# Kernel optimization log

Hardware: AMD Instinct MI355X
Metric: run time of the kernel (lower is better)

The kernel has to match this reference:

```python
import jax, jax.numpy as jnp
import numpy as np

EPS = 1e-3  # keras LayerNormalization default epsilon

def _ln(x, gamma, beta):
    m = jnp.mean(x, axis=-1, keepdims=True)
    v = jnp.var(x, axis=-1, keepdims=True)
    return gamma * (x - m) * jax.lax.rsqrt(v + EPS) + beta

def setup_inputs() -> dict:
    B, T, F, H = 256, 128, 4, 512  # T*F must equal H (skip-connection constraint in context GRN)
    D = T * F
    key = jax.random.key(0)
    ks = jax.random.split(key, 16)
    s = lambda fan: 1.0 / np.sqrt(fan)
    inp = {
        "inputs": jax.random.normal(ks[0], (B, T, F), jnp.float32),
        # context GRN (input dim D = T*F = H)
        "W1c": jax.random.normal(ks[1], (D, H), jnp.float32) * s(D),
        "b1c": jnp.zeros((H,), jnp.float32),
        "W2c": jax.random.normal(ks[2], (H, H), jnp.float32) * s(H),
        "b2c": jnp.zeros((H,), jnp.float32),
        "Wgc": jax.random.normal(ks[3], (H, H), jnp.float32) * s(H),
        "bgc": jnp.zeros((H,), jnp.float32),
        "gamma_c": jnp.ones((H,), jnp.float32),
        "beta_c": jnp.zeros((H,), jnp.float32),
        # softmax variable-selection head
        "Wsel": jax.random.normal(ks[4], (H, F), jnp.float32) * s(H),
        "bsel": jnp.zeros((F,), jnp.float32),
        # F per-variable GRNs, batched over leading F axis (input dim 1)
        "w1": jax.random.normal(ks[5], (F, H), jnp.float32),
        "b1": jnp.zeros((F, H), jnp.float32),
        "W2": jax.random.normal(ks[6], (F, H, H), jnp.float32) * s(H),
        "b2": jnp.zeros((F, H), jnp.float32),
        "Wg": jax.random.normal(ks[7], (F, H, H), jnp.float32) * s(H),
        "bg": jnp.zeros((F, H), jnp.float32),
        "gamma": jnp.ones((F, H), jnp.float32),
        "beta": jnp.zeros((F, H), jnp.float32),
    }
    return inp

def reference(inputs, W1c, b1c, W2c, b2c, Wgc, bgc, gamma_c, beta_c,
              Wsel, bsel, w1, b1, W2, b2, Wg, bg, gamma, beta):
    B, T, F = inputs.shape
    # ---- context GRN on flattened inputs (skip == flat since T*F == H) ----
    flat = inputs.reshape(B, T * F)
    x = jax.nn.elu(flat @ W1c + b1c)
    x = x @ W2c + b2c
    g = jax.nn.sigmoid(x @ Wgc + bgc)
    ctx = _ln(g * x + (1.0 - g) * flat, gamma_c, beta_c)
    # ---- softmax selection weights over variables ----
    sel = jax.nn.softmax(ctx @ Wsel + bsel)  # [B, F]
    # ---- per-variable GRNs, batched over F (input is scalar per variable) ----
    v = inputs[..., None]                              # [B,T,F,1] (skip path)
    x1 = jax.nn.elu(v * w1 + b1)                       # [B,T,F,H]
    x2 = jnp.einsum('btfh,fhk->btfk', x1, W2) + b2     # dense2
    gv = jax.nn.sigmoid(jnp.einsum('btfh,fhk->btfk', x2, Wg) + bg)
    gated = gv * x2 + (1.0 - gv) * v                   # skip broadcasts [B,T,F,1]
    tv = _ln(gated, gamma, beta)                       # [B,T,F,H]
    # ---- weighted sum over variables ----
    selected = jnp.einsum('btfh,bf->bth', tv, sel)     # [B,T,H]
    sel_weights = jnp.tile(sel[:, None, None, :], (1, T, 1, 1))  # [B,T,1,F]
    return selected, sel_weights
```

## Files before the change

kernel.cpp:

```cpp
#include <hip/hip_runtime.h>
#include <math.h>


#define H 512
#define NF 4
#define MTOT 32768

typedef unsigned short u16;
typedef unsigned int u32;
typedef __attribute__((ext_vector_type(8))) short short8;
typedef __attribute__((ext_vector_type(4))) float f32x4;
typedef __attribute__((ext_vector_type(4))) u32 u32x4;

__device__ __forceinline__ u16 f2bf(float x) {
  union { float f; u32 u; } v; v.f = x;
  return (u16)((v.u + 0x7fffu + ((v.u >> 16) & 1u)) >> 16);
}
__device__ __forceinline__ float bf2f(u32 h16) {
  union { u32 u; float f; } v; v.u = h16 << 16;
  return v.f;
}
__device__ __forceinline__ float elu_f(float x) {
  return x > 0.0f ? x : (__expf(x) - 1.0f);
}
__device__ __forceinline__ float sigmoid_f(float x) {
  return __builtin_amdgcn_rcpf(1.0f + __expf(-x));
}
__device__ __forceinline__ u32 cvtpk(float lo, float hi) {
  u32 r;
  asm("v_cvt_pk_bf16_f32 %0, %1, %2" : "=v"(r) : "v"(lo), "v"(hi));
  return r;
}
template <int CTRL>
__device__ __forceinline__ float dppadd(float v) {
  int t = __builtin_amdgcn_update_dpp(0, __float_as_int(v), CTRL, 0xF, 0xF, true);
  return v + __int_as_float(t);
}
__device__ __forceinline__ float red16(float v) {
  v = dppadd<0xB1>(v);
  v = dppadd<0x4E>(v);
  v = dppadd<0x141>(v);
  v = dppadd<0x140>(v);
  return v;
}

__device__ __forceinline__ void glld16(const void* g, void* l) {
  __builtin_amdgcn_global_load_lds(
      (const __attribute__((address_space(1))) u32*)(unsigned long long)(uintptr_t)g,
      (__attribute__((address_space(3))) u32*)(u32)(uintptr_t)l, 16, 0, 0);
}

#define MFMA16(a, b, c) __builtin_amdgcn_mfma_f32_16x16x32_bf16((a), (b), (c), 0, 0, 0)

__global__ __launch_bounds__(256)
void pack_weights(const float* __restrict__ W2, const float* __restrict__ Wg,
                  const float* __restrict__ W1c, const float* __restrict__ W2c,
                  const float* __restrict__ Wgc,
                  u16* __restrict__ W2p, u16* __restrict__ Wgp, u16* __restrict__ Cp) {
  int g = blockIdx.x * 256 + threadIdx.x;
  int r = g & 32767; int mat = g >> 15;
  if (mat >= 11) return;
  int lane = r & 63, nt = (r >> 6) & 31, kk = (r >> 11) & 15;
  const float* src; u16* dst;
  if (mat < 4)      { src = W2 + (size_t)mat * 262144;       dst = W2p + (size_t)mat * 262144; }
  else if (mat < 8) { src = Wg + (size_t)(mat - 4) * 262144; dst = Wgp + (size_t)(mat - 4) * 262144; }
  else              { src = (mat == 8 ? W1c : (mat == 9 ? W2c : Wgc));
                      dst = Cp + (size_t)(mat - 8) * 262144; }
  dst += (((size_t)kk * 32 + nt) * 64 + lane) * 8;
  int n  = nt * 16 + (lane & 15);
  int k0 = kk * 32 + (lane >> 4) * 8;
  short8 pk;
  #pragma unroll
  for (int j = 0; j < 8; ++j) pk[j] = (short)f2bf(src[(size_t)(k0 + j) * H + n]);
  *(short8*)dst = pk;
}

struct TileCtx {
  int tid, wid, lane, quad, col;
};


template <bool PREFETCH_TAIL>
__device__ __forceinline__ void gemm_kloop(const TileCtx& c, const u16* Wp,
                                           const u16* nextWp,
                                           u16* sA, u16* sB0, u16* sB1,
                                           f32x4 acc[4][2]) {
  #pragma unroll 1
  for (int kk = 0; kk < 16; ++kk) {
    if (kk < 15) {
      const u16* src = Wp + (kk + 1) * 16384 + c.tid * 8;
      u16* dst = (((kk + 1) & 1) ? sB1 : sB0) + c.tid * 8;
      glld16(src, dst);
      glld16(src + 8192, dst + 8192);
    } else if (PREFETCH_TAIL) {
      const u16* src = nextWp + c.tid * 8;
      glld16(src, sB0 + c.tid * 8);
      glld16(src + 8192, sB0 + c.tid * 8 + 8192);
    }
    const u16* bp = ((kk & 1) ? sB1 : sB0) + c.wid * 1024 + c.lane * 8;
    short8 bb0 = *(const short8*)(bp);
    short8 bb1 = *(const short8*)(bp + 512);
    const int kq = kk * 4 + c.quad;
    const int s0 = (kq ^ (c.col & 7)) * 8;
    short8 a0 = *(const short8*)&sA[(     c.col) * 512 + s0];
    short8 a1 = *(const short8*)&sA[(16 + c.col) * 512 + s0];
    short8 a2 = *(const short8*)&sA[(32 + c.col) * 512 + s0];
    short8 a3 = *(const short8*)&sA[(48 + c.col) * 512 + s0];
    acc[0][0] = MFMA16(a0, bb0, acc[0][0]); acc[0][1] = MFMA16(a0, bb1, acc[0][1]);
    acc[1][0] = MFMA16(a1, bb0, acc[1][0]); acc[1][1] = MFMA16(a1, bb1, acc[1][1]);
    acc[2][0] = MFMA16(a2, bb0, acc[2][0]); acc[2][1] = MFMA16(a2, bb1, acc[2][1]);
    acc[3][0] = MFMA16(a3, bb0, acc[3][0]); acc[3][1] = MFMA16(a3, bb1, acc[3][1]);
    __syncthreads();
  }
}

__device__ __forceinline__ void store_x2_pair(const TileCtx& c, u16* sA,
                                              int mt, int nt, u32 o01, u32 o23) {
  const bool even = (c.lane & 1) == 0;
  const u32 send = even ? o23 : o01;
  const u32 recv = (u32)__builtin_amdgcn_update_dpp(0, (int)send, 0xB1, 0xF, 0xF, true);
  const u32 hi = even ? recv : o23;
  const u32 lo = even ? o01 : recv;
  const u32 dlo = __builtin_amdgcn_perm(hi, lo, 0x05040100u);
  const u32 dhi = __builtin_amdgcn_perm(hi, lo, 0x07060302u);
  const int n  = c.wid * 32 + nt * 16 + c.col;
  const int np = n & ~1;
  const int mA = mt * 16 + c.quad * 4 + (even ? 0 : 2);
  const int iA = mA * 512 + ((((np >> 3) ^ (mA & 7)) << 3) + (np & 7));
  const int mB = mA + 1;
  const int iB = mB * 512 + ((((np >> 3) ^ (mB & 7)) << 3) + (np & 7));
  *(u32*)&sA[iA] = dlo;
  *(u32*)&sA[iB] = dhi;
}

__device__ __forceinline__ void ln_reduce(const TileCtx& c, float* sRedF,
                                          f32x4 acc[4][2]) {
  #pragma unroll
  for (int mt = 0; mt < 4; ++mt) {
    float rs[4], rq[4];
    #pragma unroll
    for (int reg = 0; reg < 4; ++reg) {
      rs[reg] = 0.f; rq[reg] = 0.f;
      #pragma unroll
      for (int nt = 0; nt < 2; ++nt) {
        const float gt = acc[mt][nt][reg];
        rs[reg] += gt; rq[reg] += gt * gt;
      }
      rs[reg] = red16(rs[reg]);
      rq[reg] = red16(rq[reg]);
    }
    if (c.col == 0) {
      #pragma unroll
      for (int reg = 0; reg < 4; ++reg) {
        const int m = mt * 16 + c.quad * 4 + reg;
        float2 sq; sq.x = rs[reg]; sq.y = rq[reg];
        *(float2*)&sRedF[m * 36 + c.wid * 2] = sq;
      }
    }
  }
  __syncthreads();
  if (c.tid < 64) {
    const int row = c.tid;
    float s = 0.f, q = 0.f;
    #pragma unroll
    for (int jj = 0; jj < 8; ++jj) {
      float4 v = *(float4*)&sRedF[row * 36 + jj * 4];
      s += v.x + v.z; q += v.y + v.w;
    }
    const float mu = s * (1.0f / H);
    const float rstd = rsqrtf(q * (1.0f / H) - mu * mu + 1e-3f);
    float2 mr; mr.x = mu; mr.y = rstd;
    *(float2*)&sRedF[2304 + row * 2] = mr;
  }
  __syncthreads();
}

__global__ __launch_bounds__(1024)
void ctx_mfma(const float* __restrict__ in,
              const u16* __restrict__ Cp,
              const float* __restrict__ b1c, const float* __restrict__ b2c,
              const float* __restrict__ bgc,
              const float* __restrict__ gamma_c, const float* __restrict__ beta_c,
              const float* __restrict__ Wsel, const float* __restrict__ bsel,
              float* __restrict__ sel_ws,
              float* __restrict__ selw_out)
{
  __shared__ __align__(16) u16 smem[65536];
  u16* const sA  = smem;
  u16* const sB0 = smem + 32768;
  u16* const sB1 = smem + 49152;
  float* const sRedF = (float*)smem;
  float* const sZ   = (float*)sB0;
  float* const sSel = (float*)sB0 + 1024;

  TileCtx c;
  c.tid = threadIdx.x; c.wid = c.tid >> 6; c.lane = c.tid & 63;
  c.quad = c.lane >> 4; c.col = c.lane & 15;
  const int b0 = blockIdx.x * 64;
  const u16* W1cp = Cp;
  const u16* W2cp = Cp + 262144;
  const u16* Wgcp = Cp + 524288;

  glld16(W1cp + c.tid * 8, sB0 + c.tid * 8);
  glld16(W1cp + c.tid * 8 + 8192, sB0 + c.tid * 8 + 8192);

  {
    const int m = c.tid >> 4;
    const int kb = (c.tid & 15) * 32;
    const float* rowp = in + (size_t)(b0 + m) * H;
    #pragma unroll
    for (int gg = 0; gg < 4; ++gg) {
      const int ge = (gg + (c.tid & 15)) & 3;
      const int k = kb + ge * 8;
      float4 v0 = *(const float4*)&rowp[k];
      float4 v1 = *(const float4*)&rowp[k + 4];
      u32x4 pk4;
      pk4.x = cvtpk(v0.x, v0.y);
      pk4.y = cvtpk(v0.z, v0.w);
      pk4.z = cvtpk(v1.x, v1.y);
      pk4.w = cvtpk(v1.z, v1.w);
      const int grp = (k >> 3) ^ (m & 7);
      *(u32x4*)&sA[m * 512 + grp * 8] = pk4;
    }
  }
  __syncthreads();

  f32x4 acc[4][2];
  #pragma unroll
  for (int mt = 0; mt < 4; ++mt) { acc[mt][0] = (f32x4){0,0,0,0}; acc[mt][1] = (f32x4){0,0,0,0}; }

  gemm_kloop<true>(c, W1cp, W2cp, sA, sB0, sB1, acc);
  {
    float bv[2] = { b1c[c.wid * 32 + c.col], b1c[c.wid * 32 + 16 + c.col] };
    #pragma unroll
    for (int mt = 0; mt < 4; ++mt)
      #pragma unroll
      for (int nt = 0; nt < 2; ++nt) {
        const u32 o01 = cvtpk(elu_f(acc[mt][nt][0] + bv[nt]), elu_f(acc[mt][nt][1] + bv[nt]));
        const u32 o23 = cvtpk(elu_f(acc[mt][nt][2] + bv[nt]), elu_f(acc[mt][nt][3] + bv[nt]));
        store_x2_pair(c, sA, mt, nt, o01, o23);
      }
  }
  __syncthreads();

  float xr[4][2][4];
  #pragma unroll
  for (int mt = 0; mt < 4; ++mt) { acc[mt][0] = (f32x4){0,0,0,0}; acc[mt][1] = (f32x4){0,0,0,0}; }
  gemm_kloop<true>(c, W2cp, Wgcp, sA, sB0, sB1, acc);
  {
    float bv[2] = { b2c[c.wid * 32 + c.col], b2c[c.wid * 32 + 16 + c.col] };
    #pragma unroll
    for (int mt = 0; mt < 4; ++mt)
      #pragma unroll
      for (int nt = 0; nt < 2; ++nt) {
        #pragma unroll
        for (int reg = 0; reg < 4; ++reg) xr[mt][nt][reg] = acc[mt][nt][reg] + bv[nt];
        const u32 o01 = cvtpk(xr[mt][nt][0], xr[mt][nt][1]);
        const u32 o23 = cvtpk(xr[mt][nt][2], xr[mt][nt][3]);
        store_x2_pair(c, sA, mt, nt, o01, o23);
      }
  }
  __syncthreads();

  #pragma unroll
  for (int mt = 0; mt < 4; ++mt) { acc[mt][0] = (f32x4){0,0,0,0}; acc[mt][1] = (f32x4){0,0,0,0}; }
  gemm_kloop<false>(c, Wgcp, nullptr, sA, sB0, sB1, acc);
  {
    float bv[2] = { bgc[c.wid * 32 + c.col], bgc[c.wid * 32 + 16 + c.col] };
    #pragma unroll
    for (int mt = 0; mt < 4; ++mt)
      #pragma unroll
      for (int nt = 0; nt < 2; ++nt) {
        const int n = c.wid * 32 + nt * 16 + c.col;
        #pragma unroll
        for (int reg = 0; reg < 4; ++reg) {
          const int m = mt * 16 + c.quad * 4 + reg;
          const float fl = in[(size_t)(b0 + m) * H + n];
          const float gv = sigmoid_f(acc[mt][nt][reg] + bv[nt]);
          acc[mt][nt][reg] = gv * xr[mt][nt][reg] + (1.0f - gv) * fl;
        }
      }
  }
  ln_reduce(c, sRedF, acc);
  {
    float gm[2], bt[2];
    #pragma unroll
    for (int nt = 0; nt < 2; ++nt) {
      const int n = c.wid * 32 + nt * 16 + c.col;
      gm[nt] = gamma_c[n]; bt[nt] = beta_c[n];
    }
    u16 cv[4][2][4];
    #pragma unroll
    for (int mt = 0; mt < 4; ++mt)
      #pragma unroll
      for (int reg = 0; reg < 4; ++reg) {
        const int m = mt * 16 + c.quad * 4 + reg;
        float2 mr = *(float2*)&sRedF[2304 + m * 2];
        #pragma unroll
        for (int nt = 0; nt < 2; ++nt)
          cv[mt][nt][reg] = f2bf(gm[nt] * ((acc[mt][nt][reg] - mr.x) * mr.y) + bt[nt]);
      }
    __syncthreads();
    #pragma unroll
    for (int mt = 0; mt < 4; ++mt)
      #pragma unroll
      for (int reg = 0; reg < 4; ++reg) {
        const int m = mt * 16 + c.quad * 4 + reg;
        #pragma unroll
        for (int nt = 0; nt < 2; ++nt)
          sA[m * 512 + c.wid * 32 + nt * 16 + c.col] = cv[mt][nt][reg];
      }
  }
  __syncthreads();

  {
    const int r = c.tid >> 4, fq = (c.tid >> 2) & 3, p = c.tid & 3;
    float z = 0.f;
    const u16* rowp = &sA[r * 512 + p * 128];
    const float* wp = Wsel + (size_t)p * 128 * NF + fq;
    #pragma unroll 8
    for (int h = 0; h < 128; ++h) z += bf2f(rowp[h]) * wp[h * NF];
    sZ[((r * 4 + fq) << 2) + p] = z;
  }
  __syncthreads();
  if (c.tid < 64) {
    const int r = c.tid;
    float zz[4];
    #pragma unroll
    for (int ff = 0; ff < 4; ++ff) {
      float4 v = *(float4*)&sZ[(r * 4 + ff) << 2];
      zz[ff] = v.x + v.y + v.z + v.w + bsel[ff];
    }
    float mx = fmaxf(fmaxf(zz[0], zz[1]), fmaxf(zz[2], zz[3]));
    float e0 = __expf(zz[0]-mx), e1 = __expf(zz[1]-mx), e2 = __expf(zz[2]-mx), e3 = __expf(zz[3]-mx);
    float inv = __builtin_amdgcn_rcpf(e0 + e1 + e2 + e3);
    sSel[r*4]   = e0*inv; sSel[r*4+1] = e1*inv;
    sSel[r*4+2] = e2*inv; sSel[r*4+3] = e3*inv;
  }
  __syncthreads();
  if (c.tid < 256) {
    const int r = c.tid >> 2, f = c.tid & 3;
    sel_ws[(b0 + r) * NF + f] = sSel[r * 4 + f];
  }
  {
    const int m = c.tid >> 4;
    const int jb = (c.tid & 15) * 32;
    float s0 = sSel[m*4], s1 = sSel[m*4+1], s2 = sSel[m*4+2], s3 = sSel[m*4+3];
    float4 v; v.x = s0; v.y = s1; v.z = s2; v.w = s3;
    #pragma unroll
    for (int j = 0; j < 8; ++j)
      *(float4*)&selw_out[(size_t)(b0 + m) * H + jb + j * 4] = v;
  }
}


__device__ __forceinline__ void stage_chunk8(int tid, const u16* src, u16* dst) {
  glld16(src + tid * 8,         dst + tid * 8);
  glld16(src + tid * 8 + 4096,  dst + tid * 8 + 4096);
  glld16(src + tid * 8 + 8192,  dst + tid * 8 + 8192);
  glld16(src + tid * 8 + 12288, dst + tid * 8 + 12288);
}

template <bool PREFETCH_TAIL>
__device__ __forceinline__ void gemm_kloop8(const TileCtx& c, const u16* Wp,
                                            const u16* nextWp,
                                            u16* sA, u16* sB0, u16* sB1,
                                            f32x4 acc[4][4]) {
  #pragma unroll 1
  for (int kk = 0; kk < 16; ++kk) {
    if (kk < 15) {
      stage_chunk8(c.tid, Wp + (kk + 1) * 16384, (((kk + 1) & 1) ? sB1 : sB0));
    } else if (PREFETCH_TAIL) {
      stage_chunk8(c.tid, nextWp, sB0);
    }
    const u16* bp = ((kk & 1) ? sB1 : sB0) + c.wid * 2048 + c.lane * 8;
    short8 bb[4];
    #pragma unroll
    for (int nt = 0; nt < 4; ++nt) bb[nt] = *(const short8*)(bp + nt * 512);
    const int kq = kk * 4 + c.quad;
    const int s0 = (kq ^ (c.col & 7)) * 8;
    #pragma unroll
    for (int mt = 0; mt < 4; ++mt) {
      short8 a = *(const short8*)&sA[(mt * 16 + c.col) * 512 + s0];
      #pragma unroll
      for (int nt = 0; nt < 4; ++nt)
        acc[mt][nt] = MFMA16(a, bb[nt], acc[mt][nt]);
    }
    __syncthreads();
  }
}

__device__ __forceinline__ void store_x2_pair_n(const TileCtx& c, u16* sA,
                                                int mt, int n, u32 o01, u32 o23) {
  const bool even = (c.lane & 1) == 0;
  const u32 send = even ? o23 : o01;
  const u32 recv = (u32)__builtin_amdgcn_update_dpp(0, (int)send, 0xB1, 0xF, 0xF, true);
  const u32 hi = even ? recv : o23;
  const u32 lo = even ? o01 : recv;
  const u32 dlo = __builtin_amdgcn_perm(hi, lo, 0x05040100u);
  const u32 dhi = __builtin_amdgcn_perm(hi, lo, 0x07060302u);
  const int np = n & ~1;
  const int mA = mt * 16 + c.quad * 4 + (even ? 0 : 2);
  const int iA = mA * 512 + ((((np >> 3) ^ (mA & 7)) << 3) + (np & 7));
  const int mB = mA + 1;
  const int iB = mB * 512 + ((((np >> 3) ^ (mB & 7)) << 3) + (np & 7));
  *(u32*)&sA[iA] = dlo;
  *(u32*)&sA[iB] = dhi;
}

__device__ __forceinline__ void ln_reduce8(const TileCtx& c, float* sRedF,
                                           f32x4 acc[4][4]) {
  #pragma unroll
  for (int mt = 0; mt < 4; ++mt) {
    float rs[4], rq[4];
    #pragma unroll
    for (int reg = 0; reg < 4; ++reg) {
      rs[reg] = 0.f; rq[reg] = 0.f;
      #pragma unroll
      for (int nt = 0; nt < 4; ++nt) {
        const float gt = acc[mt][nt][reg];
        rs[reg] += gt; rq[reg] += gt * gt;
      }
      rs[reg] = red16(rs[reg]);
      rq[reg] = red16(rq[reg]);
    }
    if (c.col == 0) {
      #pragma unroll
      for (int reg = 0; reg < 4; ++reg) {
        const int m = mt * 16 + c.quad * 4 + reg;
        float2 sq; sq.x = rs[reg]; sq.y = rq[reg];
        *(float2*)&sRedF[m * 20 + c.wid * 2] = sq;
      }
    }
  }
  __syncthreads();
  if (c.tid < 64) {
    const int row = c.tid;
    float s = 0.f, q = 0.f;
    #pragma unroll
    for (int jj = 0; jj < 4; ++jj) {
      float4 v = *(float4*)&sRedF[row * 20 + jj * 4];
      s += v.x + v.z; q += v.y + v.w;
    }
    const float mu = s * (1.0f / H);
    const float rstd = rsqrtf(q * (1.0f / H) - mu * mu + 1e-3f);
    float2 mr; mr.x = mu; mr.y = rstd;
    *(float2*)&sRedF[1280 + row * 2] = mr;
  }
  __syncthreads();
}

__global__ __launch_bounds__(512, 2)
void vsn_mfma(const float* __restrict__ in,
              const float* __restrict__ w1, const float* __restrict__ b1,
              const float* __restrict__ b2, const float* __restrict__ bg,
              const float* __restrict__ gamma, const float* __restrict__ beta,
              const u16* __restrict__ W2p, const u16* __restrict__ Wgp,
              const float* __restrict__ sel_ws,
              float* __restrict__ out)
{
  __shared__ __align__(16) u16 smem[65536];
  u16* const sA  = smem;
  u16* const sB0 = smem + 32768;
  u16* const sB1 = smem + 49152;
  float* const sRedF = (float*)smem;

  TileCtx c;
  c.tid = threadIdx.x; c.wid = c.tid >> 6; c.lane = c.tid & 63;
  c.quad = c.lane >> 4; c.col = c.lane & 15;
  const int row0 = blockIdx.x * 64;
  const int bidx = row0 >> 7;

  f32x4 outacc[4][4];
  #pragma unroll
  for (int mt = 0; mt < 4; ++mt)
    #pragma unroll
    for (int nt = 0; nt < 4; ++nt) outacc[mt][nt] = (f32x4){0,0,0,0};

  stage_chunk8(c.tid, W2p, sB0);

  #pragma unroll 1
  for (int f = 0; f < NF; ++f) {
    const u16* W2f = W2p + (size_t)f * 262144;
    const u16* Wgf = Wgp + (size_t)f * 262144;
    const u16* W2n = W2p + (size_t)((f + 1) & 3) * 262144;

    {
      const int m  = c.tid >> 3;
      const int kb = (c.tid & 7) * 64;
      const float v = in[(size_t)(row0 + m) * NF + f];
      const float* w1f = w1 + f * H;
      const float* b1f = b1 + f * H;
      #pragma unroll
      for (int gg = 0; gg < 8; ++gg) {
        const int ge = (gg + (c.tid & 7)) & 7;
        const int k = kb + ge * 8;
        float4 wv0 = *(const float4*)&w1f[k];
        float4 wv1 = *(const float4*)&w1f[k + 4];
        float4 bv0 = *(const float4*)&b1f[k];
        float4 bv1 = *(const float4*)&b1f[k + 4];
        u32x4 pk4;
        pk4.x = cvtpk(elu_f(fmaf(v, wv0.x, bv0.x)), elu_f(fmaf(v, wv0.y, bv0.y)));
        pk4.y = cvtpk(elu_f(fmaf(v, wv0.z, bv0.z)), elu_f(fmaf(v, wv0.w, bv0.w)));
        pk4.z = cvtpk(elu_f(fmaf(v, wv1.x, bv1.x)), elu_f(fmaf(v, wv1.y, bv1.y)));
        pk4.w = cvtpk(elu_f(fmaf(v, wv1.z, bv1.z)), elu_f(fmaf(v, wv1.w, bv1.w)));
        const int grp = (k >> 3) ^ (m & 7);
        *(u32x4*)&sA[m * 512 + grp * 8] = pk4;
      }
    }
    __syncthreads();

    f32x4 acc[4][4];
    #pragma unroll
    for (int mt = 0; mt < 4; ++mt)
      #pragma unroll
      for (int nt = 0; nt < 4; ++nt) acc[mt][nt] = (f32x4){0,0,0,0};

    gemm_kloop8<true>(c, W2f, Wgf, sA, sB0, sB1, acc);

    u32 x2p[4][4][2];
    {
      float bv[4];
      #pragma unroll
      for (int nt = 0; nt < 4; ++nt) bv[nt] = b2[f * H + c.wid * 64 + nt * 16 + c.col];
      #pragma unroll
      for (int mt = 0; mt < 4; ++mt)
        #pragma unroll
        for (int nt = 0; nt < 4; ++nt) {
          const u32 o01 = cvtpk(acc[mt][nt][0] + bv[nt], acc[mt][nt][1] + bv[nt]);
          const u32 o23 = cvtpk(acc[mt][nt][2] + bv[nt], acc[mt][nt][3] + bv[nt]);
          x2p[mt][nt][0] = o01; x2p[mt][nt][1] = o23;
          store_x2_pair_n(c, sA, mt, c.wid * 64 + nt * 16 + c.col, o01, o23);
        }
    }
    __syncthreads();

    #pragma unroll
    for (int mt = 0; mt < 4; ++mt)
      #pragma unroll
      for (int nt = 0; nt < 4; ++nt) acc[mt][nt] = (f32x4){0,0,0,0};
    gemm_kloop8<true>(c, Wgf, W2n, sA, sB0, sB1, acc);

    {
      const float selw = sel_ws[bidx * NF + f];
      float bv[4];
      #pragma unroll
      for (int nt = 0; nt < 4; ++nt) bv[nt] = bg[f * H + c.wid * 64 + nt * 16 + c.col];
      #pragma unroll
      for (int mt = 0; mt < 4; ++mt) {
        float vr[4];
        #pragma unroll
        for (int reg = 0; reg < 4; ++reg)
          vr[reg] = in[(size_t)(row0 + mt * 16 + c.quad * 4 + reg) * NF + f];
        #pragma unroll
        for (int nt = 0; nt < 4; ++nt)
          #pragma unroll
          for (int reg = 0; reg < 4; ++reg) {
            const u32 w = x2p[mt][nt][reg >> 1];
            const float x2v = bf2f((reg & 1) ? (w >> 16) : (w & 0xffffu));
            const float gv = sigmoid_f(acc[mt][nt][reg] + bv[nt]);
            acc[mt][nt][reg] = gv * x2v + (1.0f - gv) * vr[reg];
          }
      }
      ln_reduce8(c, sRedF, acc);
      float gm[4], bt[4];
      #pragma unroll
      for (int nt = 0; nt < 4; ++nt) {
        const int n = f * H + c.wid * 64 + nt * 16 + c.col;
        gm[nt] = gamma[n]; bt[nt] = beta[n];
      }
      #pragma unroll
      for (int mt = 0; mt < 4; ++mt)
        #pragma unroll
        for (int reg = 0; reg < 4; ++reg) {
          const int m = mt * 16 + c.quad * 4 + reg;
          float2 mr = *(float2*)&sRedF[1280 + m * 2];
          #pragma unroll
          for (int nt = 0; nt < 4; ++nt) {
            const float tv = gm[nt] * ((acc[mt][nt][reg] - mr.x) * mr.y) + bt[nt];
            outacc[mt][nt][reg] = fmaf(selw, tv, outacc[mt][nt][reg]);
          }
        }
      __syncthreads();
    }
  }

  #pragma unroll
  for (int mt = 0; mt < 4; ++mt)
    #pragma unroll
    for (int reg = 0; reg < 4; ++reg) {
      const int m = row0 + mt * 16 + c.quad * 4 + reg;
      #pragma unroll
      for (int nt = 0; nt < 4; ++nt)
        out[(size_t)m * H + c.wid * 64 + nt * 16 + c.col] = outacc[mt][nt][reg];
    }
}

extern "C" void kernel_launch(void* const* d_in, const int* in_sizes, int n_in,
                              void* d_out, int out_size, void* d_ws, size_t ws_size,
                              hipStream_t stream) {
  const float* in_     = (const float*)d_in[0];
  const float* W1c     = (const float*)d_in[1];
  const float* b1c     = (const float*)d_in[2];
  const float* W2c     = (const float*)d_in[3];
  const float* b2c     = (const float*)d_in[4];
  const float* Wgc     = (const float*)d_in[5];
  const float* bgc     = (const float*)d_in[6];
  const float* gamma_c = (const float*)d_in[7];
  const float* beta_c  = (const float*)d_in[8];
  const float* Wsel    = (const float*)d_in[9];
  const float* bsel    = (const float*)d_in[10];
  const float* w1      = (const float*)d_in[11];
  const float* b1v     = (const float*)d_in[12];
  const float* W2      = (const float*)d_in[13];
  const float* b2v     = (const float*)d_in[14];
  const float* Wg      = (const float*)d_in[15];
  const float* bgv     = (const float*)d_in[16];
  const float* gma     = (const float*)d_in[17];
  const float* bta     = (const float*)d_in[18];

  float* out_sel = (float*)d_out;
  float* out_w   = (float*)d_out + (size_t)MTOT * H;

  float* sel_ws = (float*)d_ws;
  u16*   W2p    = (u16*)((char*)d_ws + 4096);
  u16*   Wgp    = W2p + (size_t)NF * H * H;
  u16*   Cp     = Wgp + (size_t)NF * H * H;

  hipLaunchKernelGGL(pack_weights, dim3(1408), dim3(256), 0, stream,
                     W2, Wg, W1c, W2c, Wgc, W2p, Wgp, Cp);
  hipLaunchKernelGGL(ctx_mfma, dim3(4), dim3(1024), 0, stream,
                     in_, Cp, b1c, b2c, bgc, gamma_c, beta_c,
                     Wsel, bsel, sel_ws, out_w);
  hipLaunchKernelGGL(vsn_mfma, dim3(MTOT / 64), dim3(512), 0, stream,
                     in_, w1, b1v, b2v, bgv, gma, bta, W2p, Wgp, sel_ws, out_sel);
}
```

Measured before the change: 440.2 us.

## Split context GRN into per-GEMM kernels spread across more blocks

The single 4-block context kernel, which ran three chained GEMMs serially with 1024 threads per block, is split into three kernels. The first two GEMMs each run on 32 blocks, with each block owning a 64-column slab of weights, and write bf16 intermediates to global memory. The gate GEMM, LayerNorm and softmax selection run in a 512-thread kernel, and the selection logits are now computed from registers via DPP reductions. Weight packing is split into separate ctx and vsn kernels, with a slab-friendly layout for the ctx matrices. This exposes more parallelism on the small serial context stage, at the cost of extra launches and global round trips for the intermediates.

```diff
diff --git a/kernel.cpp b/kernel.cpp
--- a/kernel.cpp
+++ b/kernel.cpp
@@ -52,21 +52,24 @@
 
 #define MFMA16(a, b, c) __builtin_amdgcn_mfma_f32_16x16x32_bf16((a), (b), (c), 0, 0, 0)
 
+__device__ __forceinline__ int sA_idx(int m, int n) {
+  return m * 512 + ((((n >> 3) ^ (m & 7)) << 3) + (n & 7));
+}
+
+struct TileCtx {
+  int tid, wid, lane, quad, col;
+};
+
 __global__ __launch_bounds__(256)
-void pack_weights(const float* __restrict__ W2, const float* __restrict__ Wg,
-                  const float* __restrict__ W1c, const float* __restrict__ W2c,
-                  const float* __restrict__ Wgc,
-                  u16* __restrict__ W2p, u16* __restrict__ Wgp, u16* __restrict__ Cp) {
+void pack_vsn(const float* __restrict__ W2, const float* __restrict__ Wg,
+              u16* __restrict__ W2p, u16* __restrict__ Wgp) {
   int g = blockIdx.x * 256 + threadIdx.x;
   int r = g & 32767; int mat = g >> 15;
-  if (mat >= 11) return;
   int lane = r & 63, nt = (r >> 6) & 31, kk = (r >> 11) & 15;
   const float* src; u16* dst;
-  if (mat < 4)      { src = W2 + (size_t)mat * 262144;       dst = W2p + (size_t)mat * 262144; }
-  else if (mat < 8) { src = Wg + (size_t)(mat - 4) * 262144; dst = Wgp + (size_t)(mat - 4) * 262144; }
-  else              { src = (mat == 8 ? W1c : (mat == 9 ? W2c : Wgc));
-                      dst = Cp + (size_t)(mat - 8) * 262144; }
-  dst += (((size_t)kk * 32 + nt) * 64 + lane) * 8;
+  if (mat < 4) { src = W2 + (size_t)mat * 262144;       dst = W2p + (size_t)mat * 262144; }
+  else         { src = Wg + (size_t)(mat - 4) * 262144; dst = Wgp + (size_t)(mat - 4) * 262144; }
+  dst += (size_t)r * 8;
   int n  = nt * 16 + (lane & 15);
   int k0 = kk * 32 + (lane >> 4) * 8;
   short8 pk;
@@ -75,282 +78,151 @@
   *(short8*)dst = pk;
 }
 
-struct TileCtx {
-  int tid, wid, lane, quad, col;
-};
-
-
-template <bool PREFETCH_TAIL>
-__device__ __forceinline__ void gemm_kloop(const TileCtx& c, const u16* Wp,
-                                           const u16* nextWp,
+__global__ __launch_bounds__(256)
+void pack_ctx(const float* __restrict__ W1c, const float* __restrict__ W2c,
+              const float* __restrict__ Wgc, u16* __restrict__ Cp) {
+  int g = blockIdx.x * 256 + threadIdx.x;
+  int r = g & 32767; int mat = g >> 15;
+  const float* src = (mat == 0) ? W1c : (mat == 1) ? W2c : Wgc;
+  u16* dst = Cp + (size_t)mat * 262144 + (size_t)r * 8;
+  int lane = r & 63;
+  int n, k0;
+  if (mat < 2) {
+    int nb = r >> 12, kk = (r >> 8) & 15, ntg = (r >> 6) & 3;
+    n  = nb * 64 + ntg * 16 + (lane & 15);
+    k0 = kk * 32 + (lane >> 4) * 8;
+  } else {
+    int nt = (r >> 6) & 31, kk = (r >> 11) & 15;
+    n  = nt * 16 + (lane & 15);
+    k0 = kk * 32 + (lane >> 4) * 8;
+  }
+  short8 pk;
+  #pragma unroll
+  for (int j = 0; j < 8; ++j) pk[j] = (short)f2bf(src[(size_t)(k0 + j) * H + n]);
+  *(short8*)dst = pk;
+}
+
+
+__device__ __forceinline__ void slab_kloop(const TileCtx& c, const u16* Wslab,
                                            u16* sA, u16* sB0, u16* sB1,
-                                           f32x4 acc[4][2]) {
+                                           f32x4 acc[4]) {
   #pragma unroll 1
   for (int kk = 0; kk < 16; ++kk) {
-    if (kk < 15) {
-      const u16* src = Wp + (kk + 1) * 16384 + c.tid * 8;
-      u16* dst = (((kk + 1) & 1) ? sB1 : sB0) + c.tid * 8;
-      glld16(src, dst);
-      glld16(src + 8192, dst + 8192);
-    } else if (PREFETCH_TAIL) {
-      const u16* src = nextWp + c.tid * 8;
-      glld16(src, sB0 + c.tid * 8);
-      glld16(src + 8192, sB0 + c.tid * 8 + 8192);
-    }
-    const u16* bp = ((kk & 1) ? sB1 : sB0) + c.wid * 1024 + c.lane * 8;
-    short8 bb0 = *(const short8*)(bp);
-    short8 bb1 = *(const short8*)(bp + 512);
+    if (kk < 15)
+      glld16(Wslab + (kk + 1) * 2048 + c.tid * 8,
+             (((kk + 1) & 1) ? sB1 : sB0) + c.tid * 8);
+    const u16* bp = ((kk & 1) ? sB1 : sB0) + c.wid * 512 + c.lane * 8;
+    short8 bb = *(const short8*)(bp);
     const int kq = kk * 4 + c.quad;
     const int s0 = (kq ^ (c.col & 7)) * 8;
     short8 a0 = *(const short8*)&sA[(     c.col) * 512 + s0];
     short8 a1 = *(const short8*)&sA[(16 + c.col) * 512 + s0];
     short8 a2 = *(const short8*)&sA[(32 + c.col) * 512 + s0];
     short8 a3 = *(const short8*)&sA[(48 + c.col) * 512 + s0];
-    acc[0][0] = MFMA16(a0, bb0, acc[0][0]); acc[0][1] = MFMA16(a0, bb1, acc[0][1]);
-    acc[1][0] = MFMA16(a1, bb0, acc[1][0]); acc[1][1] = MFMA16(a1, bb1, acc[1][1]);
-    acc[2][0] = MFMA16(a2, bb0, acc[2][0]); acc[2][1] = MFMA16(a2, bb1, acc[2][1]);
-    acc[3][0] = MFMA16(a3, bb0, acc[3][0]); acc[3][1] = MFMA16(a3, bb1, acc[3][1]);
+    acc[0] = MFMA16(a0, bb, acc[0]);
+    acc[1] = MFMA16(a1, bb, acc[1]);
+    acc[2] = MFMA16(a2, bb, acc[2]);
+    acc[3] = MFMA16(a3, bb, acc[3]);
     __syncthreads();
   }
 }
 
-__device__ __forceinline__ void store_x2_pair(const TileCtx& c, u16* sA,
-                                              int mt, int nt, u32 o01, u32 o23) {
-  const bool even = (c.lane & 1) == 0;
-  const u32 send = even ? o23 : o01;
-  const u32 recv = (u32)__builtin_amdgcn_update_dpp(0, (int)send, 0xB1, 0xF, 0xF, true);
-  const u32 hi = even ? recv : o23;
-  const u32 lo = even ? o01 : recv;
-  const u32 dlo = __builtin_amdgcn_perm(hi, lo, 0x05040100u);
-  const u32 dhi = __builtin_amdgcn_perm(hi, lo, 0x07060302u);
-  const int n  = c.wid * 32 + nt * 16 + c.col;
-  const int np = n & ~1;
-  const int mA = mt * 16 + c.quad * 4 + (even ? 0 : 2);
-  const int iA = mA * 512 + ((((np >> 3) ^ (mA & 7)) << 3) + (np & 7));
-  const int mB = mA + 1;
-  const int iB = mB * 512 + ((((np >> 3) ^ (mB & 7)) << 3) + (np & 7));
-  *(u32*)&sA[iA] = dlo;
-  *(u32*)&sA[iB] = dhi;
-}
-
-__device__ __forceinline__ void ln_reduce(const TileCtx& c, float* sRedF,
-                                          f32x4 acc[4][2]) {
-  #pragma unroll
-  for (int mt = 0; mt < 4; ++mt) {
-    float rs[4], rq[4];
-    #pragma unroll
-    for (int reg = 0; reg < 4; ++reg) {
-      rs[reg] = 0.f; rq[reg] = 0.f;
-      #pragma unroll
-      for (int nt = 0; nt < 2; ++nt) {
-        const float gt = acc[mt][nt][reg];
-        rs[reg] += gt; rq[reg] += gt * gt;
-      }
-      rs[reg] = red16(rs[reg]);
-      rq[reg] = red16(rq[reg]);
-    }
-    if (c.col == 0) {
-      #pragma unroll
-      for (int reg = 0; reg < 4; ++reg) {
-        const int m = mt * 16 + c.quad * 4 + reg;
-        float2 sq; sq.x = rs[reg]; sq.y = rq[reg];
-        *(float2*)&sRedF[m * 36 + c.wid * 2] = sq;
-      }
-    }
-  }
-  __syncthreads();
-  if (c.tid < 64) {
-    const int row = c.tid;
-    float s = 0.f, q = 0.f;
-    #pragma unroll
-    for (int jj = 0; jj < 8; ++jj) {
-      float4 v = *(float4*)&sRedF[row * 36 + jj * 4];
-      s += v.x + v.z; q += v.y + v.w;
-    }
-    const float mu = s * (1.0f / H);
-    const float rstd = rsqrtf(q * (1.0f / H) - mu * mu + 1e-3f);
-    float2 mr; mr.x = mu; mr.y = rstd;
-    *(float2*)&sRedF[2304 + row * 2] = mr;
-  }
-  __syncthreads();
-}
-
-__global__ __launch_bounds__(1024)
-void ctx_mfma(const float* __restrict__ in,
-              const u16* __restrict__ Cp,
-              const float* __restrict__ b1c, const float* __restrict__ b2c,
-              const float* __restrict__ bgc,
-              const float* __restrict__ gamma_c, const float* __restrict__ beta_c,
-              const float* __restrict__ Wsel, const float* __restrict__ bsel,
-              float* __restrict__ sel_ws,
-              float* __restrict__ selw_out)
-{
-  __shared__ __align__(16) u16 smem[65536];
+__global__ __launch_bounds__(256)
+void ctx_g1(const float* __restrict__ in, const u16* __restrict__ Cp,
+            const float* __restrict__ b1c, u16* __restrict__ x1g) {
+  __shared__ __align__(16) u16 smem[36864];
   u16* const sA  = smem;
   u16* const sB0 = smem + 32768;
-  u16* const sB1 = smem + 49152;
-  float* const sRedF = (float*)smem;
-  float* const sZ   = (float*)sB0;
-  float* const sSel = (float*)sB0 + 1024;
-
+  u16* const sB1 = smem + 34816;
   TileCtx c;
   c.tid = threadIdx.x; c.wid = c.tid >> 6; c.lane = c.tid & 63;
   c.quad = c.lane >> 4; c.col = c.lane & 15;
-  const int b0 = blockIdx.x * 64;
-  const u16* W1cp = Cp;
-  const u16* W2cp = Cp + 262144;
-  const u16* Wgcp = Cp + 524288;
-
-  glld16(W1cp + c.tid * 8, sB0 + c.tid * 8);
-  glld16(W1cp + c.tid * 8 + 8192, sB0 + c.tid * 8 + 8192);
+  const int mb = blockIdx.x >> 3, nb = blockIdx.x & 7;
+  const int m0 = mb * 64;
+  const u16* Wslab = Cp + (size_t)nb * 32768;
+
+  glld16(Wslab + c.tid * 8, sB0 + c.tid * 8);
 
   {
-    const int m = c.tid >> 4;
-    const int kb = (c.tid & 15) * 32;
-    const float* rowp = in + (size_t)(b0 + m) * H;
-    #pragma unroll
-    for (int gg = 0; gg < 4; ++gg) {
-      const int ge = (gg + (c.tid & 15)) & 3;
+    const int m = c.tid >> 2;
+    const int kb = (c.tid & 3) * 128;
+    const float* rowp = in + (size_t)(m0 + m) * H;
+    #pragma unroll
+    for (int gg = 0; gg < 16; ++gg) {
+      const int ge = (gg + (c.tid & 3) * 4) & 15;
       const int k = kb + ge * 8;
       float4 v0 = *(const float4*)&rowp[k];
       float4 v1 = *(const float4*)&rowp[k + 4];
       u32x4 pk4;
-      pk4.x = cvtpk(v0.x, v0.y);
-      pk4.y = cvtpk(v0.z, v0.w);
-      pk4.z = cvtpk(v1.x, v1.y);
-      pk4.w = cvtpk(v1.z, v1.w);
+      pk4.x = cvtpk(v0.x, v0.y); pk4.y = cvtpk(v0.z, v0.w);
+      pk4.z = cvtpk(v1.x, v1.y); pk4.w = cvtpk(v1.z, v1.w);
       const int grp = (k >> 3) ^ (m & 7);
       *(u32x4*)&sA[m * 512 + grp * 8] = pk4;
     }
   }
   __syncthreads();
 
-  f32x4 acc[4][2];
-  #pragma unroll
-  for (int mt = 0; mt < 4; ++mt) { acc[mt][0] = (f32x4){0,0,0,0}; acc[mt][1] = (f32x4){0,0,0,0}; }
-
-  gemm_kloop<true>(c, W1cp, W2cp, sA, sB0, sB1, acc);
+  f32x4 acc[4];
+  #pragma unroll
+  for (int mt = 0; mt < 4; ++mt) acc[mt] = (f32x4){0,0,0,0};
+  slab_kloop(c, Wslab, sA, sB0, sB1, acc);
+
+  const int n = nb * 64 + c.wid * 16 + c.col;
+  const float bv = b1c[n];
+  #pragma unroll
+  for (int mt = 0; mt < 4; ++mt)
+    #pragma unroll
+    for (int reg = 0; reg < 4; ++reg) {
+      const int m = m0 + mt * 16 + c.quad * 4 + reg;
+      x1g[(size_t)m * H + n] = f2bf(elu_f(acc[mt][reg] + bv));
+    }
+}
+
+__global__ __launch_bounds__(256)
+void ctx_g2(const u16* __restrict__ x1g, const u16* __restrict__ Cp,
+            const float* __restrict__ b2c, u16* __restrict__ xg) {
+  __shared__ __align__(16) u16 smem[36864];
+  u16* const sA  = smem;
+  u16* const sB0 = smem + 32768;
+  u16* const sB1 = smem + 34816;
+  TileCtx c;
+  c.tid = threadIdx.x; c.wid = c.tid >> 6; c.lane = c.tid & 63;
+  c.quad = c.lane >> 4; c.col = c.lane & 15;
+  const int mb = blockIdx.x >> 3, nb = blockIdx.x & 7;
+  const int m0 = mb * 64;
+  const u16* Wslab = Cp + 262144 + (size_t)nb * 32768;
+
+  glld16(Wslab + c.tid * 8, sB0 + c.tid * 8);
+
   {
-    float bv[2] = { b1c[c.wid * 32 + c.col], b1c[c.wid * 32 + 16 + c.col] };
-    #pragma unroll
-    for (int mt = 0; mt < 4; ++mt)
-      #pragma unroll
-      for (int nt = 0; nt < 2; ++nt) {
-        const u32 o01 = cvtpk(elu_f(acc[mt][nt][0] + bv[nt]), elu_f(acc[mt][nt][1] + bv[nt]));
-        const u32 o23 = cvtpk(elu_f(acc[mt][nt][2] + bv[nt]), elu_f(acc[mt][nt][3] + bv[nt]));
-        store_x2_pair(c, sA, mt, nt, o01, o23);
-      }
-  }
-  __syncthreads();
-
-  float xr[4][2][4];
-  #pragma unroll
-  for (int mt = 0; mt < 4; ++mt) { acc[mt][0] = (f32x4){0,0,0,0}; acc[mt][1] = (f32x4){0,0,0,0}; }
-  gemm_kloop<true>(c, W2cp, Wgcp, sA, sB0, sB1, acc);
-  {
-    float bv[2] = { b2c[c.wid * 32 + c.col], b2c[c.wid * 32 + 16 + c.col] };
-    #pragma unroll
-    for (int mt = 0; mt < 4; ++mt)
-      #pragma unroll
-      for (int nt = 0; nt < 2; ++nt) {
-        #pragma unroll
-        for (int reg = 0; reg < 4; ++reg) xr[mt][nt][reg] = acc[mt][nt][reg] + bv[nt];
-        const u32 o01 = cvtpk(xr[mt][nt][0], xr[mt][nt][1]);
-        const u32 o23 = cvtpk(xr[mt][nt][2], xr[mt][nt][3]);
-        store_x2_pair(c, sA, mt, nt, o01, o23);
-      }
-  }
-  __syncthreads();
-
-  #pragma unroll
-  for (int mt = 0; mt < 4; ++mt) { acc[mt][0] = (f32x4){0,0,0,0}; acc[mt][1] = (f32x4){0,0,0,0}; }
-  gemm_kloop<false>(c, Wgcp, nullptr, sA, sB0, sB1, acc);
-  {
-    float bv[2] = { bgc[c.wid * 32 + c.col], bgc[c.wid * 32 + 16 + c.col] };
-    #pragma unroll
-    for (int mt = 0; mt < 4; ++mt)
-      #pragma unroll
-      for (int nt = 0; nt < 2; ++nt) {
-        const int n = c.wid * 32 + nt * 16 + c.col;
-        #pragma unroll
-        for (int reg = 0; reg < 4; ++reg) {
-          const int m = mt * 16 + c.quad * 4 + reg;
-          const float fl = in[(size_t)(b0 + m) * H + n];
-          const float gv = sigmoid_f(acc[mt][nt][reg] + bv[nt]);
-          acc[mt][nt][reg] = gv * xr[mt][nt][reg] + (1.0f - gv) * fl;
-        }
-      }
-  }
-  ln_reduce(c, sRedF, acc);
-  {
-    float gm[2], bt[2];
-    #pragma unroll
-    for (int nt = 0; nt < 2; ++nt) {
-      const int n = c.wid * 32 + nt * 16 + c.col;
-      gm[nt] = gamma_c[n]; bt[nt] = beta_c[n];
-    }
-    u16 cv[4][2][4];
-    #pragma unroll
-    for (int mt = 0; mt < 4; ++mt)
-      #pragma unroll
-      for (int reg = 0; reg < 4; ++reg) {
-        const int m = mt * 16 + c.quad * 4 + reg;
-        float2 mr = *(float2*)&sRedF[2304 + m * 2];
-        #pragma unroll
-        for (int nt = 0; nt < 2; ++nt)
-          cv[mt][nt][reg] = f2bf(gm[nt] * ((acc[mt][nt][reg] - mr.x) * mr.y) + bt[nt]);
-      }
-    __syncthreads();
-    #pragma unroll
-    for (int mt = 0; mt < 4; ++mt)
-      #pragma unroll
-      for (int reg = 0; reg < 4; ++reg) {
-        const int m = mt * 16 + c.quad * 4 + reg;
-        #pragma unroll
-        for (int nt = 0; nt < 2; ++nt)
-          sA[m * 512 + c.wid * 32 + nt * 16 + c.col] = cv[mt][nt][reg];
-      }
-  }
-  __syncthreads();
-
-  {
-    const int r = c.tid >> 4, fq = (c.tid >> 2) & 3, p = c.tid & 3;
-    float z = 0.f;
-    const u16* rowp = &sA[r * 512 + p * 128];
-    const float* wp = Wsel + (size_t)p * 128 * NF + fq;
-    #pragma unroll 8
-    for (int h = 0; h < 128; ++h) z += bf2f(rowp[h]) * wp[h * NF];
-    sZ[((r * 4 + fq) << 2) + p] = z;
-  }
-  __syncthreads();
-  if (c.tid < 64) {
-    const int r = c.tid;
-    float zz[4];
-    #pragma unroll
-    for (int ff = 0; ff < 4; ++ff) {
-      float4 v = *(float4*)&sZ[(r * 4 + ff) << 2];
-      zz[ff] = v.x + v.y + v.z + v.w + bsel[ff];
-    }
-    float mx = fmaxf(fmaxf(zz[0], zz[1]), fmaxf(zz[2], zz[3]));
-    float e0 = __expf(zz[0]-mx), e1 = __expf(zz[1]-mx), e2 = __expf(zz[2]-mx), e3 = __expf(zz[3]-mx);
-    float inv = __builtin_amdgcn_rcpf(e0 + e1 + e2 + e3);
-    sSel[r*4]   = e0*inv; sSel[r*4+1] = e1*inv;
-    sSel[r*4+2] = e2*inv; sSel[r*4+3] = e3*inv;
-  }
-  __syncthreads();
-  if (c.tid < 256) {
-    const int r = c.tid >> 2, f = c.tid & 3;
-    sel_ws[(b0 + r) * NF + f] = sSel[r * 4 + f];
-  }
-  {
-    const int m = c.tid >> 4;
-    const int jb = (c.tid & 15) * 32;
-    float s0 = sSel[m*4], s1 = sSel[m*4+1], s2 = sSel[m*4+2], s3 = sSel[m*4+3];
-    float4 v; v.x = s0; v.y = s1; v.z = s2; v.w = s3;
-    #pragma unroll
-    for (int j = 0; j < 8; ++j)
-      *(float4*)&selw_out[(size_t)(b0 + m) * H + jb + j * 4] = v;
-  }
+    const int m = c.tid >> 2;
+    const int kb = (c.tid & 3) * 128;
+    const u16* rowp = x1g + (size_t)(m0 + m) * H;
+    #pragma unroll
+    for (int gg = 0; gg < 16; ++gg) {
+      const int ge = (gg + (c.tid & 3) * 4) & 15;
+      const int k = kb + ge * 8;
+      short8 w = *(const short8*)&rowp[k];
+      const int grp = (k >> 3) ^ (m & 7);
+      *(short8*)&sA[m * 512 + grp * 8] = w;
+    }
+  }
+  __syncthreads();
+
+  f32x4 acc[4];
+  #pragma unroll
+  for (int mt = 0; mt < 4; ++mt) acc[mt] = (f32x4){0,0,0,0};
+  slab_kloop(c, Wslab, sA, sB0, sB1, acc);
+
+  const int n = nb * 64 + c.wid * 16 + c.col;
+  const float bv = b2c[n];
+  #pragma unroll
+  for (int mt = 0; mt < 4; ++mt)
+    #pragma unroll
+    for (int reg = 0; reg < 4; ++reg) {
+      const int m = m0 + mt * 16 + c.quad * 4 + reg;
+      xg[(size_t)m * H + n] = f2bf(acc[mt][reg] + bv);
+    }
 }
 
 
@@ -448,6 +320,138 @@
     *(float2*)&sRedF[1280 + row * 2] = mr;
   }
   __syncthreads();
+}
+
+__global__ __launch_bounds__(512)
+void ctx_g3(const float* __restrict__ in, const u16* __restrict__ xg,
+            const u16* __restrict__ Cp,
+            const float* __restrict__ bgc,
+            const float* __restrict__ gamma_c, const float* __restrict__ beta_c,
+            const float* __restrict__ Wsel, const float* __restrict__ bsel,
+            float* __restrict__ sel_ws,
+            float* __restrict__ selw_out)
+{
+  __shared__ __align__(16) u16 smem[65536];
+  u16* const sA  = smem;
+  u16* const sB0 = smem + 32768;
+  u16* const sB1 = smem + 49152;
+  float* const sRedF = (float*)sB0;
+  float* const sZp   = (float*)sB0 + 2048;
+  float* const sZf   = (float*)sB0 + 4096;
+  float* const sSel  = (float*)sB0 + 4352;
+
+  TileCtx c;
+  c.tid = threadIdx.x; c.wid = c.tid >> 6; c.lane = c.tid & 63;
+  c.quad = c.lane >> 4; c.col = c.lane & 15;
+  const int b0 = blockIdx.x * 64;
+  const u16* Wgcp = Cp + 524288;
+
+  stage_chunk8(c.tid, Wgcp, sB0);
+
+  {
+    const int m  = c.tid >> 3;
+    const int kb = (c.tid & 7) * 64;
+    const u16* rowp = xg + (size_t)(b0 + m) * H;
+    #pragma unroll
+    for (int gg = 0; gg < 8; ++gg) {
+      const int ge = (gg + (c.tid & 7)) & 7;
+      const int k = kb + ge * 8;
+      short8 w = *(const short8*)&rowp[k];
+      const int grp = (k >> 3) ^ (m & 7);
+      *(short8*)&sA[m * 512 + grp * 8] = w;
+    }
+  }
+  __syncthreads();
+
+  f32x4 acc[4][4];
+  #pragma unroll
+  for (int mt = 0; mt < 4; ++mt)
+    #pragma unroll
+    for (int nt = 0; nt < 4; ++nt) acc[mt][nt] = (f32x4){0,0,0,0};
+  gemm_kloop8<false>(c, Wgcp, nullptr, sA, sB0, sB1, acc);
+
+  {
+    float bv[4];
+    #pragma unroll
+    for (int nt = 0; nt < 4; ++nt) bv[nt] = bgc[c.wid * 64 + nt * 16 + c.col];
+    #pragma unroll
+    for (int mt = 0; mt < 4; ++mt)
+      #pragma unroll
+      for (int nt = 0; nt < 4; ++nt) {
+        const int n = c.wid * 64 + nt * 16 + c.col;
+        #pragma unroll
+        for (int reg = 0; reg < 4; ++reg) {
+          const int m = mt * 16 + c.quad * 4 + reg;
+          const float xv = bf2f(sA[sA_idx(m, n)]);
+          const float fl = in[(size_t)(b0 + m) * H + n];
+          const float gv = sigmoid_f(acc[mt][nt][reg] + bv[nt]);
+          acc[mt][nt][reg] = gv * xv + (1.0f - gv) * fl;
+        }
+      }
+  }
+  __syncthreads();
+  ln_reduce8(c, sRedF, acc);
+
+  {
+    float gm[4], bt[4]; float4 ws4[4];
+    #pragma unroll
+    for (int nt = 0; nt < 4; ++nt) {
+      const int n = c.wid * 64 + nt * 16 + c.col;
+      gm[nt] = gamma_c[n]; bt[nt] = beta_c[n];
+      ws4[nt] = *(const float4*)&Wsel[n * NF];
+    }
+    #pragma unroll
+    for (int mt = 0; mt < 4; ++mt)
+      #pragma unroll
+      for (int reg = 0; reg < 4; ++reg) {
+        const int m = mt * 16 + c.quad * 4 + reg;
+        float2 mr = *(float2*)&sRedF[1280 + m * 2];
+        float zp[4] = {0.f, 0.f, 0.f, 0.f};
+        #pragma unroll
+        for (int nt = 0; nt < 4; ++nt) {
+          const float ctxv = gm[nt] * ((acc[mt][nt][reg] - mr.x) * mr.y) + bt[nt];
+          zp[0] = fmaf(ctxv, ws4[nt].x, zp[0]);
+          zp[1] = fmaf(ctxv, ws4[nt].y, zp[1]);
+          zp[2] = fmaf(ctxv, ws4[nt].z, zp[2]);
+          zp[3] = fmaf(ctxv, ws4[nt].w, zp[3]);
+        }
+        #pragma unroll
+        for (int f = 0; f < 4; ++f) zp[f] = red16(zp[f]);
+        if (c.col == 0) {
+          #pragma unroll
+          for (int f = 0; f < 4; ++f) sZp[(m * 8 + c.wid) * 4 + f] = zp[f];
+        }
+      }
+  }
+  __syncthreads();
+  if (c.tid < 256) {
+    const int m = c.tid >> 2, f = c.tid & 3;
+    float z = bsel[f];
+    #pragma unroll
+    for (int w = 0; w < 8; ++w) z += sZp[(m * 8 + w) * 4 + f];
+    sZf[m * 4 + f] = z;
+  }
+  __syncthreads();
+  if (c.tid < 64) {
+    const int m = c.tid;
+    float z0 = sZf[m*4], z1 = sZf[m*4+1], z2 = sZf[m*4+2], z3 = sZf[m*4+3];
+    float mx = fmaxf(fmaxf(z0, z1), fmaxf(z2, z3));
+    float e0 = __expf(z0-mx), e1 = __expf(z1-mx), e2 = __expf(z2-mx), e3 = __expf(z3-mx);
+    float inv = __builtin_amdgcn_rcpf(e0 + e1 + e2 + e3);
+    sSel[m*4]   = e0*inv; sSel[m*4+1] = e1*inv;
+    sSel[m*4+2] = e2*inv; sSel[m*4+3] = e3*inv;
+    sel_ws[(b0+m)*NF]   = e0*inv; sel_ws[(b0+m)*NF+1] = e1*inv;
+    sel_ws[(b0+m)*NF+2] = e2*inv; sel_ws[(b0+m)*NF+3] = e3*inv;
+  }
+  __syncthreads();
+  {
+    const int m = c.tid >> 3;
+    const int jb = (c.tid & 7) * 64;
+    float4 v; v.x = sSel[m*4]; v.y = sSel[m*4+1]; v.z = sSel[m*4+2]; v.w = sSel[m*4+3];
+    #pragma unroll
+    for (int j = 0; j < 16; ++j)
+      *(float4*)&selw_out[(size_t)(b0 + m) * H + jb + j * 4] = v;
+  }
 }
 
 __global__ __launch_bounds__(512, 2)
@@ -626,12 +630,20 @@
   u16*   W2p    = (u16*)((char*)d_ws + 4096);
   u16*   Wgp    = W2p + (size_t)NF * H * H;
   u16*   Cp     = Wgp + (size_t)NF * H * H;
-
-  hipLaunchKernelGGL(pack_weights, dim3(1408), dim3(256), 0, stream,
-                     W2, Wg, W1c, W2c, Wgc, W2p, Wgp, Cp);
-  hipLaunchKernelGGL(ctx_mfma, dim3(4), dim3(1024), 0, stream,
-                     in_, Cp, b1c, b2c, bgc, gamma_c, beta_c,
-                     Wsel, bsel, sel_ws, out_w);
+  u16*   x1g    = Cp + 3 * 262144;
+  u16*   xg     = x1g + 131072;
+
+  hipLaunchKernelGGL(pack_ctx, dim3(384), dim3(256), 0, stream,
+                     W1c, W2c, Wgc, Cp);
+  hipLaunchKernelGGL(pack_vsn, dim3(1024), dim3(256), 0, stream,
+                     W2, Wg, W2p, Wgp);
+  hipLaunchKernelGGL(ctx_g1, dim3(32), dim3(256), 0, stream,
+                     in_, Cp, b1c, x1g);
+  hipLaunchKernelGGL(ctx_g2, dim3(32), dim3(256), 0, stream,
+                     x1g, Cp, b2c, xg);
+  hipLaunchKernelGGL(ctx_g3, dim3(4), dim3(512), 0, stream,
+                     in_, xg, Cp, bgc, gamma_c, beta_c, Wsel, bsel,
+                     sel_ws, out_w);
   hipLaunchKernelGGL(vsn_mfma, dim3(MTOT / 64), dim3(512), 0, stream,
                      in_, w1, b1v, b2v, bgv, gma, bta, W2p, Wgp, sel_ws, out_sel);
 }
```

After: 427.4 us. 2.9% less time.
